# Kernel optimization log

Hardware: AMD Instinct MI355X
Metric: run time of the kernel (lower is better)

## Reference

```python
import jax, jax.numpy as jnp
import numpy as np

H = 8          # kv heads
D = 128        # head dim
EPS = 1e-6
NEG = -1e9

def rmsnorm(x, w):
    rms = jnp.sqrt(jnp.mean(x * x, axis=-1, keepdims=True) + EPS)
    return x / rms * w

def apply_rotary(x, cos, sin):
    # x: [B, h, T, D]; cos/sin: [1, 1, T, D/2]
    x1, x2 = jnp.split(x, 2, axis=-1)
    return jnp.concatenate([x1 * cos - x2 * sin, x1 * sin + x2 * cos], axis=-1)


def setup_inputs() -> dict:
    key = jax.random.key(0)
    ks = jax.random.split(key, 7)
    B, T, hid = 1, 4096, 1024
    s = 0.02
    return {
        "x":   jax.random.normal(ks[0], (B, T, hid), jnp.float32),
        "cos": jax.random.normal(ks[1], (1, 1, T, D // 2), jnp.float32),
        "sin": jax.random.normal(ks[2], (1, 1, T, D // 2), jnp.float32),
        "Wq":  jax.random.normal(ks[3], (hid, 2 * hid), jnp.float32) * s,
        "Wk":  jax.random.normal(ks[4], (hid, hid), jnp.float32) * s,
        "Wv":  jax.random.normal(ks[5], (hid, hid), jnp.float32) * s,
        "Wo":  jax.random.normal(ks[6], (2 * hid, hid), jnp.float32) * s,
        "qn_w": jnp.ones((D,), jnp.float32),
        "kn_w": jnp.ones((D,), jnp.float32),
    }


def reference(x, cos, sin, Wq, Wk, Wv, Wo, qn_w, kn_w):
    B, T, _ = x.shape
    scale = D ** -0.5

    q = (x @ Wq).reshape(B, T, 2 * H, D).transpose(0, 2, 1, 3)  # [B,2H,T,D]
    k = (x @ Wk).reshape(B, T, H, D).transpose(0, 2, 1, 3)      # [B,H,T,D]
    v = (x @ Wv).reshape(B, T, H, D).transpose(0, 2, 1, 3)      # [B,H,T,D]

    q = apply_rotary(rmsnorm(q, qn_w), cos, sin)
    k = apply_rotary(rmsnorm(k, kn_w), cos, sin)

    # GQA expand: query head i uses kv head i // 2
    k = jnp.repeat(k, 2, axis=1)  # [B,2H,T,D]
    v = jnp.repeat(v, 2, axis=1)

    attn = jnp.einsum("bhtd,bhsd->bhts", q, k) * scale
    causal = jnp.tril(jnp.ones((T, T), bool))
    attn = jnp.where(causal, attn, NEG)
    attn = jax.nn.softmax(attn, axis=-1)

    out = jnp.einsum("bhts,bhsd->bhtd", attn, v)
    out = out.transpose(0, 2, 1, 3).reshape(B, T, 2 * H * D)
    return out @ Wo
```

## Files before the change

### kernel.cpp

```cpp
#include <hip/hip_runtime.h>
#include <hip/hip_bf16.h>

#define H2 16
#define HKV 8
#define DHEAD 128
#define HID 1024
#define NQ 2048

typedef unsigned short u16;
typedef __bf16 bf16x8 __attribute__((ext_vector_type(8)));
typedef float f32x4 __attribute__((ext_vector_type(4)));

__device__ __forceinline__ u16 f2bf(float x) {
    unsigned int u = __float_as_uint(x);
    unsigned int r = (u + 0x7fffu + ((u >> 16) & 1u)) >> 16;
    return (u16)r;
}
__device__ __forceinline__ float bf2f(u16 x) {
    return __uint_as_float(((unsigned int)x) << 16);
}

__device__ __forceinline__ unsigned int pack_bf16(float hi, float lo) {
    unsigned int a = __float_as_uint(hi) + 0x8000u;
    unsigned int b = __float_as_uint(lo) + 0x8000u;
    return __builtin_amdgcn_perm(a, b, 0x07060302u);
}

__device__ __forceinline__ bf16x8 ld_frag(const u16* p) {
    bf16x8 r;
    *reinterpret_cast<uint4*>(&r) = *reinterpret_cast<const uint4*>(p);
    return r;
}

__device__ __forceinline__ void gload_lds16(const u16* g, u16* l) {
    __builtin_amdgcn_global_load_lds((const __attribute__((address_space(1))) void*)g,
                                     (__attribute__((address_space(3))) void*)l, 16, 0, 0);
}

__global__ __launch_bounds__(256) void cast_f32_bf16(const float* __restrict__ in,
                                                     u16* __restrict__ out, int n4) {
    int i = blockIdx.x * 256 + threadIdx.x;
    if (i < n4) {
        float4 v = reinterpret_cast<const float4*>(in)[i];
        ushort4 o;
        o.x = f2bf(v.x); o.y = f2bf(v.y); o.z = f2bf(v.z); o.w = f2bf(v.w);
        reinterpret_cast<ushort4*>(out)[i] = o;
    }
}

__global__ __launch_bounds__(256) void transpose_cast_all(const float* __restrict__ Wq,
                                                          const float* __restrict__ Wk,
                                                          const float* __restrict__ Wv,
                                                          const float* __restrict__ Wo,
                                                          u16* __restrict__ Wqkvb,
                                                          u16* __restrict__ Wob) {
    __shared__ u16 t[32][34];
    int bid = blockIdx.x;
    const float* in; u16* out; int K, N, k0, n0;
    if (bid < 2048) {
        in = Wq; out = Wqkvb; K = 1024; N = 2048;
        k0 = (bid & 31) * 32; n0 = (bid >> 5) * 32;
    } else if (bid < 3072) {
        int b = bid - 2048;
        in = Wk; out = Wqkvb + (size_t)2048 * 1024; K = 1024; N = 1024;
        k0 = (b & 31) * 32; n0 = (b >> 5) * 32;
    } else if (bid < 4096) {
        int b = bid - 3072;
        in = Wv; out = Wqkvb + (size_t)3072 * 1024; K = 1024; N = 1024;
        k0 = (b & 31) * 32; n0 = (b >> 5) * 32;
    } else {
        int b = bid - 4096;
        in = Wo; out = Wob; K = 2048; N = 1024;
        k0 = (b & 63) * 32; n0 = (b >> 6) * 32;
    }
    for (int c = threadIdx.x; c < 1024; c += 256) {
        int k = c >> 5, n = c & 31;
        t[k][n] = f2bf(in[(size_t)(k0 + k) * N + n0 + n]);
    }
    __syncthreads();
    for (int c = threadIdx.x; c < 1024; c += 256) {
        int n = c >> 5, k = c & 31;
        out[(size_t)(n0 + n) * K + k0 + k] = t[k][n];
    }
}

__global__ __launch_bounds__(256) void gemm_qkv_fused(const u16* __restrict__ A,
                                                      const u16* __restrict__ Bt,
                                                      const float* __restrict__ cosp,
                                                      const float* __restrict__ sinp,
                                                      const float* __restrict__ qnw,
                                                      const float* __restrict__ knw,
                                                      u16* __restrict__ Qb,
                                                      u16* __restrict__ Kb,
                                                      u16* __restrict__ Vbt,
                                                      int T, float qscale) {
    __shared__ u16 smem[16384];
    u16* Asm = smem;
    u16* Bsm = smem + 8192;
    const int K = 1024, N = 4096;
    int tid = threadIdx.x;
    int lane = tid & 63, wave = tid >> 6;
    int quad = lane >> 4, l15 = lane & 15;
    int wr = wave >> 1, wc = wave & 1;
    int m0 = blockIdx.y * 128, n0 = blockIdx.x * 128;

    f32x4 zero = {0.f, 0.f, 0.f, 0.f};
    f32x4 acc[4][4];
    for (int i = 0; i < 4; i++)
        for (int j = 0; j < 4; j++) acc[i][j] = zero;

    int r0 = 16 * wave + (lane >> 2);
    int r1 = r0 + 64;
    int ks0 = (lane & 3) ^ ((r0 >> 1) & 3);
    int ks1 = (lane & 3) ^ ((r1 >> 1) & 3);
    const u16* ga0 = A + (size_t)(m0 + r0) * K + ks0 * 8;
    const u16* ga1 = A + (size_t)(m0 + r1) * K + ks1 * 8;
    const u16* gb0 = Bt + (size_t)(n0 + r0) * K + ks0 * 8;
    const u16* gb1 = Bt + (size_t)(n0 + r1) * K + ks1 * 8;

    int swz = (quad ^ ((l15 >> 1) & 3)) * 8;

    for (int k0 = 0; k0 < K; k0 += 64) {
        __syncthreads();
        #pragma unroll
        for (int s = 0; s < 2; s++) {
            gload_lds16(ga0 + k0 + s * 32, &Asm[s * 4096 + wave * 512]);
            gload_lds16(ga1 + k0 + s * 32, &Asm[s * 4096 + (wave + 4) * 512]);
            gload_lds16(gb0 + k0 + s * 32, &Bsm[s * 4096 + wave * 512]);
            gload_lds16(gb1 + k0 + s * 32, &Bsm[s * 4096 + (wave + 4) * 512]);
        }
        __syncthreads();
        #pragma unroll
        for (int s = 0; s < 2; s++) {
            bf16x8 a[4], b[4];
            #pragma unroll
            for (int i = 0; i < 4; i++) a[i] = ld_frag(&Asm[s * 4096 + (64 * wr + 16 * i + l15) * 32 + swz]);
            #pragma unroll
            for (int j = 0; j < 4; j++) b[j] = ld_frag(&Bsm[s * 4096 + (64 * wc + 16 * j + l15) * 32 + swz]);
            #pragma unroll
            for (int i = 0; i < 4; i++)
                #pragma unroll
                for (int j = 0; j < 4; j++)
                    acc[i][j] = __builtin_amdgcn_mfma_f32_16x16x32_bf16(a[i], b[j], acc[i][j], 0, 0, 0);
        }
    }

    __syncthreads();
    u16* Ct = smem;
    #pragma unroll
    for (int i = 0; i < 4; i++) {
        int rowb = 64 * wr + 16 * i + quad * 4;
        #pragma unroll
        for (int j = 0; j < 4; j++) {
            int col = 64 * wc + 16 * j + l15;
            #pragma unroll
            for (int r = 0; r < 4; r++) {
                int row = rowb + r;
                Ct[row * 128 + (col ^ (row & 63))] = f2bf(acc[i][j][r]);
            }
        }
    }
    __syncthreads();

    if (n0 < 3072) {
        bool isq = n0 < 2048;
        int hh = isq ? (n0 >> 7) : ((n0 - 2048) >> 7);
        const float* w = isq ? qnw : knw;
        float outscale = isq ? qscale : 1.0f;
        u16* outp = isq ? (Qb + (size_t)hh * T * 128) : (Kb + (size_t)hh * T * 128);
        int d = lane;
        float wd1 = w[d], wd2 = w[d + 64];
        for (int rr = 0; rr < 32; rr++) {
            int row = wave * 32 + rr;
            int t = m0 + row;
            float v1 = bf2f(Ct[row * 128 + (d ^ (row & 63))]);
            float v2 = bf2f(Ct[row * 128 + ((d + 64) ^ (row & 63))]);
            float ss = v1 * v1 + v2 * v2;
            for (int off = 1; off < 64; off <<= 1) ss += __shfl_xor(ss, off);
            float inv = rsqrtf(ss * (1.f / 128.f) + 1e-6f);
            float n1 = v1 * inv * wd1, n2 = v2 * inv * wd2;
            float c = cosp[(size_t)t * 64 + d], s = sinp[(size_t)t * 64 + d];
            u16* orow = outp + (size_t)t * 128;
            orow[d] = f2bf((n1 * c - n2 * s) * outscale);
            orow[d + 64] = f2bf((n1 * s + n2 * c) * outscale);
        }
    } else {
        int vh = (n0 - 3072) >> 7;
        for (int dd = 0; dd < 32; dd++) {
            int dcol = wave * 32 + dd;
            u16* vrow = Vbt + ((size_t)vh * 128 + dcol) * T + m0;
            int t1 = lane, t2 = lane + 64;
            vrow[t1] = Ct[t1 * 128 + (dcol ^ (t1 & 63))];
            vrow[t2] = Ct[t2 * 128 + (dcol ^ (t2 & 63))];
        }
    }
}

__global__ __launch_bounds__(256) void gemm_bf16_n64(const u16* __restrict__ A,
                                                     const u16* __restrict__ Bt,
                                                     float* __restrict__ C,
                                                     int M, int N, int K) {
    __shared__ u16 As[2][128 * 32];
    __shared__ u16 Bs[2][64 * 32];
    int tid = threadIdx.x;
    int lane = tid & 63, wave = tid >> 6;
    int quad = lane >> 4, l15 = lane & 15;
    int m0 = blockIdx.y * 128, n0 = blockIdx.x * 64;

    f32x4 zero = {0.f, 0.f, 0.f, 0.f};
    f32x4 acc[2][4];
    for (int i = 0; i < 2; i++)
        for (int j = 0; j < 4; j++) acc[i][j] = zero;

    int ra0 = 32 * wave + (lane >> 2);
    int ra1 = ra0 + 16;
    int rb  = 16 * wave + (lane >> 2);
    int ksa0 = (lane & 3) ^ ((ra0 >> 1) & 3);
    int ksa1 = (lane & 3) ^ ((ra1 >> 1) & 3);
    int ksb  = (lane & 3) ^ ((rb >> 1) & 3);
    const u16* ga0 = A + (size_t)(m0 + ra0) * K + ksa0 * 8;
    const u16* ga1 = A + (size_t)(m0 + ra1) * K + ksa1 * 8;
    const u16* gb  = Bt + (size_t)(n0 + rb) * K + ksb * 8;

    int swz = (quad ^ ((l15 >> 1) & 3)) * 8;

    for (int k0 = 0; k0 < K; k0 += 64) {
        __syncthreads();
        #pragma unroll
        for (int s = 0; s < 2; s++) {
            gload_lds16(ga0 + k0 + s * 32, &As[s][(2 * wave) * 512]);
            gload_lds16(ga1 + k0 + s * 32, &As[s][(2 * wave + 1) * 512]);
            gload_lds16(gb + k0 + s * 32, &Bs[s][wave * 512]);
        }
        __syncthreads();
        #pragma unroll
        for (int s = 0; s < 2; s++) {
            bf16x8 a[2], b[4];
            #pragma unroll
            for (int i = 0; i < 2; i++) a[i] = ld_frag(&As[s][(32 * wave + 16 * i + l15) * 32 + swz]);
            #pragma unroll
            for (int j = 0; j < 4; j++) b[j] = ld_frag(&Bs[s][(16 * j + l15) * 32 + swz]);
            #pragma unroll
            for (int i = 0; i < 2; i++)
                #pragma unroll
                for (int j = 0; j < 4; j++)
                    acc[i][j] = __builtin_amdgcn_mfma_f32_16x16x32_bf16(a[i], b[j], acc[i][j], 0, 0, 0);
        }
    }
    for (int i = 0; i < 2; i++) {
        int rowb = m0 + 32 * wave + 16 * i + quad * 4;
        for (int j = 0; j < 4; j++) {
            int col = n0 + 16 * j + l15;
            for (int r = 0; r < 4; r++)
                C[(size_t)(rowb + r) * N + col] = acc[i][j][r];
        }
    }
}

__global__ __launch_bounds__(512, 4) void flash_attn(const u16* __restrict__ Qb,
                                                     const u16* __restrict__ Kb,
                                                     const u16* __restrict__ Vbt,
                                                     u16* __restrict__ attn, int T) {
    __shared__ u16 Ks[2][64 * 128];
    __shared__ u16 Vt[2][128 * 64];
    __shared__ u16 Ps[64 * 64];
    __shared__ float Ms[4][2][16];
    __shared__ float Ls[4][2][16];
    int tid = threadIdx.x;
    int lane = tid & 63, wave = tid >> 6;
    int qw = wave & 3, sh = wave >> 2;
    int quad = lane >> 4, l15 = lane & 15;
    int swb8 = (l15 & 7) * 8;
    int h = blockIdx.y;
    int j = (int)blockIdx.x;
    int kvh = h >> 1;

    const u16* kbase = Kb + (size_t)kvh * T * 128;
    const u16* vbase = Vbt + (size_t)kvh * 128 * T;

    int krow_ = lane >> 4;
    int kseg_ = lane & 15;
    int vrow_ = lane >> 3;
    int vseg_ = lane & 7;

    auto stage = [&](int s0, int b) {
        #pragma unroll
        for (int i = 0; i < 2; i++) {
            int ch = wave * 2 + i;
            int r = ch * 4 + krow_;
            int s = kseg_ ^ (r & 7);
            gload_lds16(kbase + (size_t)(s0 + r) * 128 + s * 8, &Ks[b][ch * 512]);
        }
        #pragma unroll
        for (int i = 0; i < 2; i++) {
            int ch = wave * 2 + i;
            int d = ch * 8 + vrow_;
            int s = vseg_ ^ (d & 7);
            gload_lds16(vbase + (size_t)d * T + s0 + s * 8, &Vt[b][ch * 512]);
        }
    };

    bf16x8 onesf;
    #pragma unroll
    for (int i = 0; i < 8; i++) onesf[i] = (__bf16)1.0f;
    f32x4 zero = {0.f, 0.f, 0.f, 0.f};
    const float L2E = 1.44269504f;

    for (int pass = 0; pass < 2; ++pass) {
        int qt = pass == 0 ? (63 - j) : j;
        int q0 = qt * 64;

        bf16x8 qf[4];
        {
            const u16* qp = Qb + ((size_t)h * T + q0 + 16 * qw + l15) * 128 + quad * 8;
            #pragma unroll
            for (int kk = 0; kk < 4; kk++) qf[kk] = ld_frag(qp + kk * 32);
        }

        float m_i = -3.0e38f;
        f32x4 lsum = zero;
        f32x4 o[8];
        for (int dt = 0; dt < 8; dt++) o[dt] = zero;

        int ntiles = qt + 1;
        stage(0, 0);
        __syncthreads();

        for (int it = 0; it < ntiles; ++it) {
            int b = it & 1;
            if (it + 1 < ntiles) stage((it + 1) * 64, 1 - b);
            bool diag = (it == qt);
            if (!(diag && sh == 1 && qw < 2)) {
                f32x4 scT[2];
                scT[0] = zero; scT[1] = zero;
                #pragma unroll
                for (int kk = 0; kk < 4; kk++)
                    #pragma unroll
                    for (int jt = 0; jt < 2; jt++) {
                        bf16x8 kfrag = ld_frag(&Ks[b][(sh * 32 + jt * 16 + l15) * 128 + ((kk * 32 + quad * 8) ^ swb8)]);
                        scT[jt] = __builtin_amdgcn_mfma_f32_16x16x32_bf16(kfrag, qf[kk], scT[jt], 0, 0, 0);
                    }

                if (diag) {
                    int qloc = 16 * qw + l15;
                    #pragma unroll
                    for (int jt = 0; jt < 2; jt++)
                        for (int r = 0; r < 4; r++)
                            if (sh * 32 + jt * 16 + quad * 4 + r > qloc) scT[jt][r] = -1e30f;
                }

                float mt = scT[0][0];
                #pragma unroll
                for (int jt = 0; jt < 2; jt++)
                    for (int r = 0; r < 4; r++) mt = fmaxf(mt, scT[jt][r]);
                mt = fmaxf(mt, __shfl_xor(mt, 16));
                mt = fmaxf(mt, __shfl_xor(mt, 32));
                float mnew = fmaxf(m_i, mt);
                float alpha = __expf(m_i - mnew);
                m_i = mnew;
                float mls = mnew * L2E;

                #pragma unroll
                for (int jt = 0; jt < 2; jt++)
                    for (int r = 0; r < 4; r++)
                        scT[jt][r] = exp2f(fmaf(scT[jt][r], L2E, -mls));

                {
                    int prow = 16 * qw + l15;
                    #pragma unroll
                    for (int jt = 0; jt < 2; jt++) {
                        int s8 = sh * 4 + 2 * jt + (quad >> 1);
                        uint2 wv;
                        wv.x = pack_bf16(scT[jt][1], scT[jt][0]);
                        wv.y = pack_bf16(scT[jt][3], scT[jt][2]);
                        *reinterpret_cast<uint2*>(&Ps[prow * 64 + (s8 ^ (l15 & 7)) * 8 + (quad & 1) * 4]) = wv;
                    }
                }

                if (__any(alpha != 1.0f)) {
                    float av[4];
                    #pragma unroll
                    for (int r = 0; r < 4; r++) av[r] = __shfl(alpha, quad * 4 + r);
                    #pragma unroll
                    for (int r = 0; r < 4; r++) lsum[r] *= av[r];
                    #pragma unroll
                    for (int dt = 0; dt < 8; dt++)
                        for (int r = 0; r < 4; r++) o[dt][r] *= av[r];
                }

                asm volatile("s_waitcnt lgkmcnt(0)" ::: "memory");

                bf16x8 pa = ld_frag(&Ps[(16 * qw + l15) * 64 + (((sh * 4 + quad) ^ (l15 & 7)) * 8)]);
                lsum = __builtin_amdgcn_mfma_f32_16x16x32_bf16(pa, onesf, lsum, 0, 0, 0);
                #pragma unroll
                for (int dt = 0; dt < 8; dt++) {
                    bf16x8 vb = ld_frag(&Vt[b][(dt * 16 + l15) * 64 + (((sh * 4 + quad) * 8) ^ swb8)]);
                    o[dt] = __builtin_amdgcn_mfma_f32_16x16x32_bf16(pa, vb, o[dt], 0, 0, 0);
                }
            }
            __syncthreads();
        }

        if (quad == 0) Ms[qw][sh][l15] = m_i;
        if (l15 == 0) {
            #pragma unroll
            for (int r = 0; r < 4; r++) Ls[qw][sh][quad * 4 + r] = lsum[r];
        }
        __syncthreads();
        float M4[4], wS[4];
        #pragma unroll
        for (int r = 0; r < 4; r++) {
            float mS = Ms[qw][sh][quad * 4 + r];
            float mO = Ms[qw][sh ^ 1][quad * 4 + r];
            M4[r] = fmaxf(mS, mO);
            wS[r] = __expf(mS - M4[r]);
        }
        float* scr = reinterpret_cast<float*>(&Ks[0][0]);
        if (sh == 1) {
            #pragma unroll
            for (int dt = 0; dt < 8; dt++)
                #pragma unroll
                for (int r = 0; r < 4; r++)
                    scr[qw * 2048 + (dt * 16 + l15) * 16 + ((quad * 4 + r) ^ l15)] = o[dt][r] * wS[r];
        }
        __syncthreads();
        if (sh == 0) {
            float inv[4];
            #pragma unroll
            for (int r = 0; r < 4; r++) {
                float mO = Ms[qw][1][quad * 4 + r];
                float wO = __expf(mO - M4[r]);
                float l = lsum[r] * wS[r] + Ls[qw][1][quad * 4 + r] * wO;
                inv[r] = 1.f / l;
            }
            #pragma unroll
            for (int dt = 0; dt < 8; dt++)
                #pragma unroll
                for (int r = 0; r < 4; r++) {
                    float val = (o[dt][r] * wS[r] +
                                 scr[qw * 2048 + (dt * 16 + l15) * 16 + ((quad * 4 + r) ^ l15)]) * inv[r];
                    int row = q0 + 16 * qw + quad * 4 + r;
                    attn[(size_t)row * NQ + h * DHEAD + dt * 16 + l15] = f2bf(val);
                }
        }
        __syncthreads();
    }
}

extern "C" void kernel_launch(void* const* d_in, const int* in_sizes, int n_in,
                              void* d_out, int out_size, void* d_ws, size_t ws_size,
                              hipStream_t stream) {
    const float* x    = (const float*)d_in[0];
    const float* cosp = (const float*)d_in[1];
    const float* sinp = (const float*)d_in[2];
    const float* Wq   = (const float*)d_in[3];
    const float* Wk   = (const float*)d_in[4];
    const float* Wv   = (const float*)d_in[5];
    const float* Wo   = (const float*)d_in[6];
    const float* qnw  = (const float*)d_in[7];
    const float* knw  = (const float*)d_in[8];
    float* out = (float*)d_out;
    const int T = in_sizes[1] / 64;

    char* ws = (char*)d_ws;
    size_t off = 0;
    auto alloc = [&](size_t bytes) {
        char* p = ws + off;
        off += (bytes + 255) & ~(size_t)255;
        return p;
    };
    u16*   xb     = (u16*)alloc((size_t)T * HID * 2);
    u16*   Wqkvb  = (u16*)alloc((size_t)4096 * HID * 2);
    u16*   Wob    = (u16*)alloc((size_t)HID * NQ * 2);
    u16*   Qb     = (u16*)alloc((size_t)H2 * T * DHEAD * 2);
    u16*   Kb     = (u16*)alloc((size_t)HKV * T * DHEAD * 2);
    u16*   Vbt    = (u16*)alloc((size_t)HKV * DHEAD * T * 2);
    u16*   attn   = (u16*)alloc((size_t)T * NQ * 2);

    cast_f32_bf16<<<(T * HID / 4 + 255) / 256, 256, 0, stream>>>(x, xb, T * HID / 4);
    transpose_cast_all<<<6144, 256, 0, stream>>>(Wq, Wk, Wv, Wo, Wqkvb, Wob);

    const float scale = 0.08838834764831845f;
    gemm_qkv_fused<<<dim3(4096 / 128, T / 128), 256, 0, stream>>>(
        xb, Wqkvb, cosp, sinp, qnw, knw, Qb, Kb, Vbt, T, scale);

    flash_attn<<<dim3(32, H2), 512, 0, stream>>>(Qb, Kb, Vbt, attn, T);

    gemm_bf16_n64<<<dim3(HID / 64, T / 128), 256, 0, stream>>>(attn, Wob, out, T, HID, NQ);
}
```

Before: 343.1 us.

## Merge prep kernels, process two rows per wave in norm-rope epilogue, deepen K step

Merges the x cast kernel and the weight transpose-cast kernel into a single launch, removing one kernel launch. In the QKV GEMM epilogue, each wave now handles two rows at once using 32-lane halves, which halves the serial row loop and shortens the shuffle reduction. The output GEMM loads 128 K values per barrier pair instead of 64, halving the syncs at the cost of double the LDS per block, which may lower occupancy.

```diff
diff --git a/kernel.cpp b/kernel.cpp
--- a/kernel.cpp
+++ b/kernel.cpp
@@ -37,25 +37,26 @@
                                      (__attribute__((address_space(3))) void*)l, 16, 0, 0);
 }
 
-__global__ __launch_bounds__(256) void cast_f32_bf16(const float* __restrict__ in,
-                                                     u16* __restrict__ out, int n4) {
-    int i = blockIdx.x * 256 + threadIdx.x;
-    if (i < n4) {
-        float4 v = reinterpret_cast<const float4*>(in)[i];
-        ushort4 o;
-        o.x = f2bf(v.x); o.y = f2bf(v.y); o.z = f2bf(v.z); o.w = f2bf(v.w);
-        reinterpret_cast<ushort4*>(out)[i] = o;
-    }
-}
-
-__global__ __launch_bounds__(256) void transpose_cast_all(const float* __restrict__ Wq,
-                                                          const float* __restrict__ Wk,
-                                                          const float* __restrict__ Wv,
-                                                          const float* __restrict__ Wo,
-                                                          u16* __restrict__ Wqkvb,
-                                                          u16* __restrict__ Wob) {
+__global__ __launch_bounds__(256) void prep_all(const float* __restrict__ x,
+                                                const float* __restrict__ Wq,
+                                                const float* __restrict__ Wk,
+                                                const float* __restrict__ Wv,
+                                                const float* __restrict__ Wo,
+                                                u16* __restrict__ xb,
+                                                u16* __restrict__ Wqkvb,
+                                                u16* __restrict__ Wob, int n4) {
     __shared__ u16 t[32][34];
     int bid = blockIdx.x;
+    if (bid >= 6144) {
+        int i = (bid - 6144) * 256 + threadIdx.x;
+        if (i < n4) {
+            float4 v = reinterpret_cast<const float4*>(x)[i];
+            ushort4 o;
+            o.x = f2bf(v.x); o.y = f2bf(v.y); o.z = f2bf(v.z); o.w = f2bf(v.w);
+            reinterpret_cast<ushort4*>(xb)[i] = o;
+        }
+        return;
+    }
     const float* in; u16* out; int K, N, k0, n0;
     if (bid < 2048) {
         in = Wq; out = Wqkvb; K = 1024; N = 2048;
@@ -97,7 +98,7 @@
     __shared__ u16 smem[16384];
     u16* Asm = smem;
     u16* Bsm = smem + 8192;
-    const int K = 1024, N = 4096;
+    const int K = 1024;
     int tid = threadIdx.x;
     int lane = tid & 63, wave = tid >> 6;
     int quad = lane >> 4, l15 = lane & 15;
@@ -168,21 +169,29 @@
         const float* w = isq ? qnw : knw;
         float outscale = isq ? qscale : 1.0f;
         u16* outp = isq ? (Qb + (size_t)hh * T * 128) : (Kb + (size_t)hh * T * 128);
-        int d = lane;
-        float wd1 = w[d], wd2 = w[d + 64];
-        for (int rr = 0; rr < 32; rr++) {
-            int row = wave * 32 + rr;
+        int l32 = lane & 31, hl = lane >> 5;
+        float w0 = w[l32], w1 = w[l32 + 32], w2 = w[l32 + 64], w3 = w[l32 + 96];
+        for (int rr = 0; rr < 16; rr++) {
+            int row = wave * 32 + rr * 2 + hl;
             int t = m0 + row;
-            float v1 = bf2f(Ct[row * 128 + (d ^ (row & 63))]);
-            float v2 = bf2f(Ct[row * 128 + ((d + 64) ^ (row & 63))]);
-            float ss = v1 * v1 + v2 * v2;
-            for (int off = 1; off < 64; off <<= 1) ss += __shfl_xor(ss, off);
+            int rx = row & 63;
+            float v0 = bf2f(Ct[row * 128 + (l32 ^ rx)]);
+            float v1 = bf2f(Ct[row * 128 + ((l32 + 32) ^ rx)]);
+            float v2 = bf2f(Ct[row * 128 + ((l32 + 64) ^ rx)]);
+            float v3 = bf2f(Ct[row * 128 + ((l32 + 96) ^ rx)]);
+            float ss = (v0 * v0 + v2 * v2) + (v1 * v1 + v3 * v3);
+            #pragma unroll
+            for (int off = 1; off < 32; off <<= 1) ss += __shfl_xor(ss, off);
             float inv = rsqrtf(ss * (1.f / 128.f) + 1e-6f);
-            float n1 = v1 * inv * wd1, n2 = v2 * inv * wd2;
-            float c = cosp[(size_t)t * 64 + d], s = sinp[(size_t)t * 64 + d];
+            float nv0 = v0 * inv * w0, nv1 = v1 * inv * w1;
+            float nv2 = v2 * inv * w2, nv3 = v3 * inv * w3;
+            float c0 = cosp[(size_t)t * 64 + l32], s0 = sinp[(size_t)t * 64 + l32];
+            float c1 = cosp[(size_t)t * 64 + l32 + 32], s1 = sinp[(size_t)t * 64 + l32 + 32];
             u16* orow = outp + (size_t)t * 128;
-            orow[d] = f2bf((n1 * c - n2 * s) * outscale);
-            orow[d + 64] = f2bf((n1 * s + n2 * c) * outscale);
+            orow[l32]      = f2bf((nv0 * c0 - nv2 * s0) * outscale);
+            orow[l32 + 64] = f2bf((nv0 * s0 + nv2 * c0) * outscale);
+            orow[l32 + 32] = f2bf((nv1 * c1 - nv3 * s1) * outscale);
+            orow[l32 + 96] = f2bf((nv1 * s1 + nv3 * c1) * outscale);
         }
     } else {
         int vh = (n0 - 3072) >> 7;
@@ -200,8 +209,8 @@
                                                      const u16* __restrict__ Bt,
                                                      float* __restrict__ C,
                                                      int M, int N, int K) {
-    __shared__ u16 As[2][128 * 32];
-    __shared__ u16 Bs[2][64 * 32];
+    __shared__ u16 As[4][128 * 32];
+    __shared__ u16 Bs[4][64 * 32];
     int tid = threadIdx.x;
     int lane = tid & 63, wave = tid >> 6;
     int quad = lane >> 4, l15 = lane & 15;
@@ -224,17 +233,17 @@
 
     int swz = (quad ^ ((l15 >> 1) & 3)) * 8;
 
-    for (int k0 = 0; k0 < K; k0 += 64) {
-        __syncthreads();
-        #pragma unroll
-        for (int s = 0; s < 2; s++) {
+    for (int k0 = 0; k0 < K; k0 += 128) {
+        __syncthreads();
+        #pragma unroll
+        for (int s = 0; s < 4; s++) {
             gload_lds16(ga0 + k0 + s * 32, &As[s][(2 * wave) * 512]);
             gload_lds16(ga1 + k0 + s * 32, &As[s][(2 * wave + 1) * 512]);
             gload_lds16(gb + k0 + s * 32, &Bs[s][wave * 512]);
         }
         __syncthreads();
         #pragma unroll
-        for (int s = 0; s < 2; s++) {
+        for (int s = 0; s < 4; s++) {
             bf16x8 a[2], b[4];
             #pragma unroll
             for (int i = 0; i < 2; i++) a[i] = ld_frag(&As[s][(32 * wave + 16 * i + l15) * 32 + swz]);
@@ -477,8 +486,8 @@
     u16*   Vbt    = (u16*)alloc((size_t)HKV * DHEAD * T * 2);
     u16*   attn   = (u16*)alloc((size_t)T * NQ * 2);
 
-    cast_f32_bf16<<<(T * HID / 4 + 255) / 256, 256, 0, stream>>>(x, xb, T * HID / 4);
-    transpose_cast_all<<<6144, 256, 0, stream>>>(Wq, Wk, Wv, Wo, Wqkvb, Wob);
+    int n4 = T * HID / 4;
+    prep_all<<<6144 + (n4 + 255) / 256, 256, 0, stream>>>(x, Wq, Wk, Wv, Wo, xb, Wqkvb, Wob, n4);
 
     const float scale = 0.08838834764831845f;
     gemm_qkv_fused<<<dim3(4096 / 128, T / 128), 256, 0, stream>>>(
```

After: 318.1 us. 1.08x faster.
